# Kernel optimization log

Measured on AMD Instinct MI355X. Metric: run time of the kernel, lower is better.

## Reference

```python
import jax, jax.numpy as jnp
import numpy as np

B, S, D = 4, 2048, 1024
H = 16
HS = D // H  # 64


def setup_inputs() -> dict:
    key = jax.random.key(0)
    ks = jax.random.split(key, 6)
    scale = 1.0 / np.sqrt(D)
    x = jax.random.normal(ks[0], (B, S, D), dtype=jnp.float32)
    # per-head projection weights, stacked: [H, D, HS]
    Wq = jax.random.normal(ks[1], (H, D, HS), dtype=jnp.float32) * scale
    Wk = jax.random.normal(ks[2], (H, D, HS), dtype=jnp.float32) * scale
    Wv = jax.random.normal(ks[3], (H, D, HS), dtype=jnp.float32) * scale
    Wo = jax.random.normal(ks[4], (D, D), dtype=jnp.float32) * scale
    bo = jax.random.normal(ks[5], (D,), dtype=jnp.float32) * 0.01
    return {"x": x, "Wq": Wq, "Wk": Wk, "Wv": Wv, "Wo": Wo, "bo": bo}


def reference(x, Wq, Wk, Wv, Wo, bo):
    # Per-head dense projections (no bias): [B,S,D] x [H,D,HS] -> [B,H,S,HS]
    q = jnp.einsum('bsd,hde->bhse', x, Wq)
    k = jnp.einsum('bsd,hde->bhse', x, Wk)
    v = jnp.einsum('bsd,hde->bhse', x, Wv)
    # scaled dot-product scores: [B,H,S,S]
    scores = jnp.einsum('bhse,bhte->bhst', q, k) / jnp.sqrt(jnp.asarray(HS, dtype=x.dtype))
    # causal mask (lower triangular kept)
    causal = jnp.tril(jnp.ones((S, S), dtype=bool))
    scores = jnp.where(causal, scores, -jnp.inf)
    attn = jax.nn.softmax(scores, axis=-1)
    # dropout is identity at inference (rate handled as 0)
    out = jnp.einsum('bhst,bhte->bhse', attn, v)  # [B,H,S,HS]
    # concat heads: [B,S,H*HS] = [B,S,D]
    out = jnp.transpose(out, (0, 2, 1, 3)).reshape(B, S, D)
    return out @ Wo + bo
```

## Files before the change

kernel.cpp:

```cpp
#include <hip/hip_runtime.h>
#include <hip/hip_bf16.h>
#include <stdint.h>

#define NB 4
#define NS 2048
#define ND 1024
#define NH 16
#define NHS 64
#define NEG_BIG (-1e30f)
#define Q_SCALE 0.18033688011112042f

typedef __bf16 bf16x8 __attribute__((ext_vector_type(8)));
typedef float floatx4 __attribute__((ext_vector_type(4)));
typedef short s16x4 __attribute__((ext_vector_type(4)));

#if defined(__has_builtin)
#if __has_builtin(__builtin_amdgcn_mfma_f32_16x16x16bf16_1k)
#define HAVE_MFMA1K 1
#endif
#endif
#ifndef HAVE_MFMA1K
#define HAVE_MFMA1K 0
#endif

static constexpr size_t WSLAB = (size_t)NH * ND * NHS;
static constexpr size_t QSLAB = (size_t)NB * NH * NS * NHS;
static constexpr size_t XSLAB = (size_t)NB * NS * ND;

__device__ __forceinline__ uint16_t f2b(float f) {
    union { __hip_bfloat16 h; uint16_t u; } cv;
    cv.h = __float2bfloat16(f);
    return cv.u;
}

__device__ __forceinline__ void gll16(const void* g, void* l) {
  __builtin_amdgcn_global_load_lds(
      (__attribute__((address_space(1))) void*)(uintptr_t)g,
      (__attribute__((address_space(3))) void*)(uintptr_t)l,
      16, 0, 0);
}

__global__ __launch_bounds__(256) void k_prep(
    const float* __restrict__ x, const float* __restrict__ Wq,
    const float* __restrict__ Wk, const float* __restrict__ Wv,
    const float* __restrict__ Wo, uint16_t* __restrict__ xb,
    uint16_t* __restrict__ wt) {
  __shared__ __align__(16) uint16_t T[64][72];
  int bid = blockIdx.x;
  int tid = threadIdx.x;
  if (bid < 4096) {
    size_t i0 = ((size_t)bid * 256 + tid) * 8;
    float4 f0 = *(const float4*)&x[i0];
    float4 f1 = *(const float4*)&x[i0 + 4];
    __align__(16) uint16_t tmp[8];
    tmp[0] = f2b(f0.x); tmp[1] = f2b(f0.y); tmp[2] = f2b(f0.z); tmp[3] = f2b(f0.w);
    tmp[4] = f2b(f1.x); tmp[5] = f2b(f1.y); tmp[6] = f2b(f1.z); tmp[7] = f2b(f1.w);
    *(uint4*)&xb[i0] = *(uint4*)tmp;
    return;
  }
  bid -= 4096;
  const float* src; uint16_t* dst;
  int srcStride, dstStride, r0, c0;
  if (bid < 768) {
    int mat = bid >> 8;
    int rem = bid & 255;
    int h = rem >> 4, dt = rem & 15;
    const float* W = (mat == 0) ? Wq : (mat == 1) ? Wk : Wv;
    src = W + (size_t)h * (ND * NHS);
    dst = wt + (size_t)mat * WSLAB + (size_t)h * (NHS * ND);
    srcStride = NHS; dstStride = ND;
    r0 = dt * 64; c0 = 0;
  } else {
    int rem = bid - 768;
    int dt = rem >> 4, et = rem & 15;
    src = Wo; dst = wt + 3 * WSLAB;
    srcStride = ND; dstStride = ND;
    r0 = dt * 64; c0 = et * 64;
  }
  for (int u = tid; u < 1024; u += 256) {
    int row = u >> 4, cq = u & 15;
    float4 f = *(const float4*)&src[(size_t)(r0 + row) * srcStride + c0 + cq * 4];
    uint16_t* p = &T[row][cq * 4];
    p[0] = f2b(f.x); p[1] = f2b(f.y); p[2] = f2b(f.z); p[3] = f2b(f.w);
  }
  __syncthreads();
  for (int u = tid; u < 512; u += 256) {
    int c = u >> 3, cg = u & 7;
    __align__(16) uint16_t tmp[8];
    for (int j = 0; j < 8; j++) tmp[j] = T[cg * 8 + j][c];
    *(uint4*)&dst[(size_t)(c0 + c) * dstStride + r0 + cg * 8] = *(uint4*)tmp;
  }
}

__global__ __launch_bounds__(512, 2) void k_qkv(
    const uint16_t* __restrict__ xb, const uint16_t* __restrict__ wt,
    uint16_t* __restrict__ qk, uint16_t* __restrict__ vt) {
  __shared__ __align__(16) uint16_t L[8 * 8704];

  int bid = blockIdx.x;
  int xcd = bid & 7, idx = bid >> 3;
  int mt = xcd * 4 + (idx & 3);
  int ntile = idx >> 2;
  int m0 = mt * 256;
  int n0 = ntile * 256;

  int tid = threadIdx.x;
  int wave = tid >> 6, lane = tid & 63, quad = lane >> 4, l16 = lane & 15;
  int wr = wave >> 2, wc = wave & 3;

  const uint16_t* pA = xb + (size_t)(m0 + (tid >> 2)) * ND + (tid & 3) * 8;
  const uint16_t* pB = wt + (size_t)(n0 + (tid >> 2)) * ND + (tid & 3) * 8;
  const int ldsStageOff = wave * 512;

  const int offA = (wr * 128 + l16) * 32 + quad * 8;
  const int offB = (wc * 64 + l16) * 32 + quad * 8;

  floatx4 acc[8][4];
  #pragma unroll
  for (int i = 0; i < 8; i++)
    #pragma unroll
    for (int j = 0; j < 4; j++) acc[i][j] = (floatx4){0.f, 0.f, 0.f, 0.f};

#define STAGE(H)                                                                \
  do {                                                                          \
    int h_ = (H);                                                               \
    if (h_ < 64) {                                                              \
      const uint16_t* g_ = ((h_ & 1) ? pB : pA) + (h_ >> 2) * 64 + ((h_ >> 1) & 1) * 32; \
      uint16_t* l_ = &L[(h_ & 7) * 8704 + ldsStageOff];                         \
      gll16(g_, l_);                                                            \
      gll16(g_ + 128 * ND, l_ + 4096);                                          \
    }                                                                           \
  } while (0)

#define PH_BAR()                         \
  do {                                   \
    asm volatile("" ::: "memory");       \
    __builtin_amdgcn_s_barrier();        \
    asm volatile("" ::: "memory");       \
  } while (0)

  STAGE(0); STAGE(1); STAGE(2); STAGE(3); STAGE(4); STAGE(5);
  asm volatile("s_waitcnt vmcnt(4)" ::: "memory");
  PH_BAR();

  bf16x8 bfr[4];

#define MFMA16(QM)                                                                                   \
  acc[(QM)*4+0][0] = __builtin_amdgcn_mfma_f32_16x16x32_bf16(af0_, bfr[0], acc[(QM)*4+0][0],0,0,0);  \
  acc[(QM)*4+0][1] = __builtin_amdgcn_mfma_f32_16x16x32_bf16(af0_, bfr[1], acc[(QM)*4+0][1],0,0,0);  \
  acc[(QM)*4+0][2] = __builtin_amdgcn_mfma_f32_16x16x32_bf16(af0_, bfr[2], acc[(QM)*4+0][2],0,0,0);  \
  acc[(QM)*4+0][3] = __builtin_amdgcn_mfma_f32_16x16x32_bf16(af0_, bfr[3], acc[(QM)*4+0][3],0,0,0);  \
  acc[(QM)*4+1][0] = __builtin_amdgcn_mfma_f32_16x16x32_bf16(af1_, bfr[0], acc[(QM)*4+1][0],0,0,0);  \
  acc[(QM)*4+1][1] = __builtin_amdgcn_mfma_f32_16x16x32_bf16(af1_, bfr[1], acc[(QM)*4+1][1],0,0,0);  \
  acc[(QM)*4+1][2] = __builtin_amdgcn_mfma_f32_16x16x32_bf16(af1_, bfr[2], acc[(QM)*4+1][2],0,0,0);  \
  acc[(QM)*4+1][3] = __builtin_amdgcn_mfma_f32_16x16x32_bf16(af1_, bfr[3], acc[(QM)*4+1][3],0,0,0);  \
  acc[(QM)*4+2][0] = __builtin_amdgcn_mfma_f32_16x16x32_bf16(af2_, bfr[0], acc[(QM)*4+2][0],0,0,0);  \
  acc[(QM)*4+2][1] = __builtin_amdgcn_mfma_f32_16x16x32_bf16(af2_, bfr[1], acc[(QM)*4+2][1],0,0,0);  \
  acc[(QM)*4+2][2] = __builtin_amdgcn_mfma_f32_16x16x32_bf16(af2_, bfr[2], acc[(QM)*4+2][2],0,0,0);  \
  acc[(QM)*4+2][3] = __builtin_amdgcn_mfma_f32_16x16x32_bf16(af2_, bfr[3], acc[(QM)*4+2][3],0,0,0);  \
  acc[(QM)*4+3][0] = __builtin_amdgcn_mfma_f32_16x16x32_bf16(af3_, bfr[0], acc[(QM)*4+3][0],0,0,0);  \
  acc[(QM)*4+3][1] = __builtin_amdgcn_mfma_f32_16x16x32_bf16(af3_, bfr[1], acc[(QM)*4+3][1],0,0,0);  \
  acc[(QM)*4+3][2] = __builtin_amdgcn_mfma_f32_16x16x32_bf16(af3_, bfr[2], acc[(QM)*4+3][2],0,0,0);  \
  acc[(QM)*4+3][3] = __builtin_amdgcn_mfma_f32_16x16x32_bf16(af3_, bfr[3], acc[(QM)*4+3][3],0,0,0)

#define PHASE(T4, KK, QM, HSTAGE, LOADB)                                        \
  {                                                                             \
    const int slA_ = (((T4) + 2 * (KK)) & 7) * 8704;                            \
    bf16x8 af0_ = *(const bf16x8*)&L[slA_ + offA + (QM) * 2048 + 0 * 512];      \
    bf16x8 af1_ = *(const bf16x8*)&L[slA_ + offA + (QM) * 2048 + 1 * 512];      \
    bf16x8 af2_ = *(const bf16x8*)&L[slA_ + offA + (QM) * 2048 + 2 * 512];      \
    bf16x8 af3_ = *(const bf16x8*)&L[slA_ + offA + (QM) * 2048 + 3 * 512];      \
    if (LOADB) {                                                                \
      const int slB_ = (((T4) + 2 * (KK) + 1) & 7) * 8704;                      \
      bfr[0] = *(const bf16x8*)&L[slB_ + offB + 0 * 512];                       \
      bfr[1] = *(const bf16x8*)&L[slB_ + offB + 1 * 512];                       \
      bfr[2] = *(const bf16x8*)&L[slB_ + offB + 2 * 512];                       \
      bfr[3] = *(const bf16x8*)&L[slB_ + offB + 3 * 512];                       \
    }                                                                           \
    STAGE(HSTAGE);                                                              \
    PH_BAR();                                                                   \
    __builtin_amdgcn_s_setprio(1);                                              \
    MFMA16(QM);                                                                 \
    __builtin_amdgcn_s_setprio(0);                                              \
  }

  for (int t = 0; t < 16; ++t) {
    int t4 = t * 4;
    PHASE(t4, 0, 0, t4 + 6, 1);
    PH_BAR();
    PHASE(t4, 0, 1, t4 + 7, 0);
    PH_BAR();
    PHASE(t4, 1, 0, t4 + 8, 1);
    PH_BAR();
    PHASE(t4, 1, 1, t4 + 9, 0);
    if (t < 14)       { asm volatile("s_waitcnt vmcnt(4)" ::: "memory"); }
    else if (t == 14) { asm volatile("s_waitcnt vmcnt(0)" ::: "memory"); }
    PH_BAR();
  }
#undef PHASE
#undef MFMA16
#undef STAGE
#undef PH_BAR

  int matid = n0 >> 10;
  if (matid == 2) {
    uint16_t* wbuf = &L[wave * 8704];
    #pragma unroll
    for (int mq = 0; mq < 8; mq++)
      #pragma unroll
      for (int nt = 0; nt < 4; nt++) {
        __align__(8) uint16_t t4v[4];
        #pragma unroll
        for (int r = 0; r < 4; r++) t4v[r] = f2b(acc[mq][nt][r]);
        int e = nt * 16 + l16;
        *(uint2*)&wbuf[e * 136 + mq * 16 + quad * 4] = *(uint2*)t4v;
      }
    __syncthreads();
    int hb = (n0 - 2048) >> 6;
    int b = m0 >> 11, s0m = m0 & 2047;
    #pragma unroll
    for (int i = 0; i < 16; i++) {
      int c = i * 512 + tid;
      int row = c >> 5, sb = c & 31;
      int hl = row >> 6, e = row & 63;
      int wsrc = (sb >> 4) * 4 + hl;
      uint4 d = *(const uint4*)&L[wsrc * 8704 + e * 136 + (sb & 15) * 8];
      *(uint4*)&vt[((size_t)(b * 16 + hb + hl) * 64 + e) * 2048 + s0m + sb * 8] = d;
    }
  } else {
    float scale = (matid == 0) ? Q_SCALE : 1.0f;
    uint16_t* base = qk + (size_t)matid * QSLAB;
    int hh = ((n0 & 1023) >> 6) + wc;
    #pragma unroll
    for (int mq = 0; mq < 8; mq++) {
      int m = m0 + wr * 128 + mq * 16 + quad * 4;
      int b = m >> 11, s = m & 2047;
      size_t rbase = ((size_t)(b * 16 + hh) * NS + s) * NHS;
      #pragma unroll
      for (int nt = 0; nt < 4; nt++)
        #pragma unroll
        for (int r = 0; r < 4; r++)
          base[rbase + (size_t)r * NHS + nt * 16 + l16] = f2b(acc[mq][nt][r] * scale);
    }
  }
}

#if HAVE_MFMA1K
__global__ __launch_bounds__(256, 4) void k_attn(
    const uint16_t* __restrict__ Q, const uint16_t* __restrict__ K,
    const uint16_t* __restrict__ VT, uint16_t* __restrict__ Y) {
  __shared__ __align__(16) uint16_t Ks[64][72];
  __shared__ __align__(16) uint16_t Vs[64][72];
  int bh = blockIdx.y;
  int b = bh >> 4, h = bh & 15;
  int ta = blockIdx.x;
  int tb = 31 - ta;
  const uint16_t* Qp = Q + (size_t)bh * (NS * NHS);
  const uint16_t* Kp = K + (size_t)bh * (NS * NHS);
  const uint16_t* Vp = VT + (size_t)bh * (NS * NHS);
  int tid = threadIdx.x;
  int wv = tid >> 6, lane = tid & 63, quad = lane >> 4, l16 = lane & 15;

  int row0 = tid >> 3, cg0 = tid & 7;
  int row1 = (tid + 256) >> 3, cg1 = tid & 7;

  int rA = ta * 64 + wv * 16 + l16;
  int rB = tb * 64 + wv * 16 + l16;
  bf16x8 aqA0 = *(const bf16x8*)&Qp[(size_t)rA * NHS + quad * 8];
  bf16x8 aqA1 = *(const bf16x8*)&Qp[(size_t)rA * NHS + 32 + quad * 8];
  bf16x8 aqB0 = *(const bf16x8*)&Qp[(size_t)rB * NHS + quad * 8];
  bf16x8 aqB1 = *(const bf16x8*)&Qp[(size_t)rB * NHS + 32 + quad * 8];

  float lAs = 0.f, lBs = 0.f;
  floatx4 oA[4], oB[4];
  for (int et = 0; et < 4; et++) {
    oA[et] = (floatx4){0.f, 0.f, 0.f, 0.f};
    oB[et] = (floatx4){0.f, 0.f, 0.f, 0.f};
  }

  uint4 rk0, rk1, rv0, rv1;
  rk0 = *(const uint4*)&Kp[(size_t)(0 * 64 + row0) * NHS + cg0 * 8];
  rk1 = *(const uint4*)&Kp[(size_t)(0 * 64 + row1) * NHS + cg1 * 8];
  rv0 = *(const uint4*)&Vp[(size_t)row0 * NS + 0 * 64 + cg0 * 8];
  rv1 = *(const uint4*)&Vp[(size_t)row1 * NS + 0 * 64 + cg1 * 8];

  for (int kt = 0; kt <= tb; kt++) {
    bool doA = (kt <= ta);
    __syncthreads();
    *(uint4*)&Ks[row0][cg0 * 8] = rk0;
    *(uint4*)&Ks[row1][cg1 * 8] = rk1;
    *(uint4*)&Vs[row0][cg0 * 8] = rv0;
    *(uint4*)&Vs[row1][cg1 * 8] = rv1;
    __syncthreads();
    if (kt < tb) {
      rk0 = *(const uint4*)&Kp[(size_t)((kt + 1) * 64 + row0) * NHS + cg0 * 8];
      rk1 = *(const uint4*)&Kp[(size_t)((kt + 1) * 64 + row1) * NHS + cg1 * 8];
      rv0 = *(const uint4*)&Vp[(size_t)row0 * NS + (kt + 1) * 64 + cg0 * 8];
      rv1 = *(const uint4*)&Vp[(size_t)row1 * NS + (kt + 1) * 64 + cg1 * 8];
    }

    s16x4 pbA[4], pbB[4];
    for (int ct = 0; ct < 4; ct++) {
      bf16x8 kb0 = *(const bf16x8*)&Ks[ct * 16 + l16][quad * 8];
      bf16x8 kb1 = *(const bf16x8*)&Ks[ct * 16 + l16][32 + quad * 8];
      int key = kt * 64 + ct * 16 + quad * 4;
      floatx4 c = (floatx4){0.f, 0.f, 0.f, 0.f};
      c = __builtin_amdgcn_mfma_f32_16x16x32_bf16(kb0, aqB0, c, 0, 0, 0);
      c = __builtin_amdgcn_mfma_f32_16x16x32_bf16(kb1, aqB1, c, 0, 0, 0);
      for (int r = 0; r < 4; r++) {
        float s = (kt == tb && key + r > rB) ? NEG_BIG : c[r];
        float p = __builtin_amdgcn_exp2f(s);
        lBs += p;
        pbB[ct][r] = (short)f2b(p);
      }
      if (doA) {
        floatx4 d = (floatx4){0.f, 0.f, 0.f, 0.f};
        d = __builtin_amdgcn_mfma_f32_16x16x32_bf16(kb0, aqA0, d, 0, 0, 0);
        d = __builtin_amdgcn_mfma_f32_16x16x32_bf16(kb1, aqA1, d, 0, 0, 0);
        for (int r = 0; r < 4; r++) {
          float s = (kt == ta && key + r > rA) ? NEG_BIG : d[r];
          float p = __builtin_amdgcn_exp2f(s);
          lAs += p;
          pbA[ct][r] = (short)f2b(p);
        }
      }
    }
    for (int et = 0; et < 4; et++)
      for (int ct = 0; ct < 4; ct++) {
        s16x4 va = *(const s16x4*)&Vs[et * 16 + l16][ct * 16 + quad * 4];
        oB[et] = __builtin_amdgcn_mfma_f32_16x16x16bf16_1k(va, pbB[ct], oB[et], 0, 0, 0);
        if (doA)
          oA[et] = __builtin_amdgcn_mfma_f32_16x16x16bf16_1k(va, pbA[ct], oA[et], 0, 0, 0);
      }
  }
  lAs += __shfl_xor(lAs, 16, 64); lAs += __shfl_xor(lAs, 32, 64);
  lBs += __shfl_xor(lBs, 16, 64); lBs += __shfl_xor(lBs, 32, 64);
  float invA = 1.f / lAs, invB = 1.f / lBs;
  uint16_t* yb = Y + (size_t)b * NS * ND + (size_t)h * NHS;
  for (int et = 0; et < 4; et++) {
    __align__(8) uint16_t tA[4], tB[4];
    for (int r = 0; r < 4; r++) {
      tA[r] = f2b(oA[et][r] * invA);
      tB[r] = f2b(oB[et][r] * invB);
    }
    *(uint2*)&yb[(size_t)rA * ND + et * 16 + quad * 4] = *(uint2*)tA;
    *(uint2*)&yb[(size_t)rB * ND + et * 16 + quad * 4] = *(uint2*)tB;
  }
}
#else
__global__ __launch_bounds__(256) void k_attn(
    const uint16_t* __restrict__ Q, const uint16_t* __restrict__ K,
    const uint16_t* __restrict__ VT, uint16_t* __restrict__ Y) {
  __shared__ __align__(16) uint16_t Ks[64][72];
  __shared__ __align__(16) uint16_t Vs[64][72];
  __shared__ __align__(16) uint16_t Ps[4][2][16][72];
  int bh = blockIdx.y;
  int b = bh >> 4, h = bh & 15;
  int ta = blockIdx.x;
  int tb = 31 - ta;
  const uint16_t* Qp = Q + (size_t)bh * (NS * NHS);
  const uint16_t* Kp = K + (size_t)bh * (NS * NHS);
  const uint16_t* Vp = VT + (size_t)bh * (NS * NHS);
  int tid = threadIdx.x;
  int wv = tid >> 6, lane = tid & 63, quad = lane >> 4, l16 = lane & 15;

  int rA = ta * 64 + wv * 16 + l16;
  int rB = tb * 64 + wv * 16 + l16;
  bf16x8 aqA0 = *(const bf16x8*)&Qp[(size_t)rA * NHS + quad * 8];
  bf16x8 aqA1 = *(const bf16x8*)&Qp[(size_t)rA * NHS + 32 + quad * 8];
  bf16x8 aqB0 = *(const bf16x8*)&Qp[(size_t)rB * NHS + quad * 8];
  bf16x8 aqB1 = *(const bf16x8*)&Qp[(size_t)rB * NHS + 32 + quad * 8];

  float lA[4] = {0.f, 0.f, 0.f, 0.f}, lB[4] = {0.f, 0.f, 0.f, 0.f};
  floatx4 oA[4], oB[4];
  for (int ct = 0; ct < 4; ct++) {
    oA[ct] = (floatx4){0.f, 0.f, 0.f, 0.f};
    oB[ct] = (floatx4){0.f, 0.f, 0.f, 0.f};
  }
  for (int kt = 0; kt <= tb; kt++) {
    bool doA = (kt <= ta);
    __syncthreads();
    for (int u = tid; u < 512; u += 256) {
      int row = u >> 3, cg = u & 7;
      *(uint4*)&Ks[row][cg * 8] =
          *(const uint4*)&Kp[(size_t)(kt * 64 + row) * NHS + cg * 8];
    }
    for (int u = tid; u < 512; u += 256) {
      int row = u >> 3, cg = u & 7;
      *(uint4*)&Vs[row][cg * 8] =
          *(const uint4*)&Vp[(size_t)row * NS + kt * 64 + cg * 8];
    }
    __syncthreads();
    floatx4 sA[4], sB[4];
    for (int ct = 0; ct < 4; ct++) {
      bf16x8 kb0 = *(const bf16x8*)&Ks[ct * 16 + l16][quad * 8];
      bf16x8 kb1 = *(const bf16x8*)&Ks[ct * 16 + l16][32 + quad * 8];
      floatx4 c = (floatx4){0.f, 0.f, 0.f, 0.f};
      c = __builtin_amdgcn_mfma_f32_16x16x32_bf16(aqB0, kb0, c, 0, 0, 0);
      c = __builtin_amdgcn_mfma_f32_16x16x32_bf16(aqB1, kb1, c, 0, 0, 0);
      sB[ct] = c;
      if (doA) {
        floatx4 d = (floatx4){0.f, 0.f, 0.f, 0.f};
        d = __builtin_amdgcn_mfma_f32_16x16x32_bf16(aqA0, kb0, d, 0, 0, 0);
        d = __builtin_amdgcn_mfma_f32_16x16x32_bf16(aqA1, kb1, d, 0, 0, 0);
        sA[ct] = d;
      }
    }
    if (kt == tb) {
      int qrb = tb * 64 + wv * 16 + quad * 4;
      for (int ct = 0; ct < 4; ct++) {
        int kg = kt * 64 + ct * 16 + l16;
        for (int r = 0; r < 4; r++)
          sB[ct][r] = (kg <= qrb + r) ? sB[ct][r] : NEG_BIG;
      }
    }
    if (doA && kt == ta) {
      int qrb = ta * 64 + wv * 16 + quad * 4;
      for (int ct = 0; ct < 4; ct++) {
        int kg = kt * 64 + ct * 16 + l16;
        for (int r = 0; r < 4; r++)
          sA[ct][r] = (kg <= qrb + r) ? sA[ct][r] : NEG_BIG;
      }
    }
    for (int ct = 0; ct < 4; ct++)
      for (int r = 0; r < 4; r++) {
        float p = __builtin_amdgcn_exp2f(sB[ct][r]);
        lB[r] += p;
        Ps[wv][1][quad * 4 + r][ct * 16 + l16] = f2b(p);
      }
    if (doA)
      for (int ct = 0; ct < 4; ct++)
        for (int r = 0; r < 4; r++) {
          float p = __builtin_amdgcn_exp2f(sA[ct][r]);
          lA[r] += p;
          Ps[wv][0][quad * 4 + r][ct * 16 + l16] = f2b(p);
        }
    bf16x8 apB0 = *(const bf16x8*)&Ps[wv][1][l16][quad * 8];
    bf16x8 apB1 = *(const bf16x8*)&Ps[wv][1][l16][32 + quad * 8];
    bf16x8 apA0, apA1;
    if (doA) {
      apA0 = *(const bf16x8*)&Ps[wv][0][l16][quad * 8];
      apA1 = *(const bf16x8*)&Ps[wv][0][l16][32 + quad * 8];
    }
    for (int ct = 0; ct < 4; ct++) {
      bf16x8 vb0 = *(const bf16x8*)&Vs[ct * 16 + l16][quad * 8];
      bf16x8 vb1 = *(const bf16x8*)&Vs[ct * 16 + l16][32 + quad * 8];
      oB[ct] = __builtin_amdgcn_mfma_f32_16x16x32_bf16(apB0, vb0, oB[ct], 0, 0, 0);
      oB[ct] = __builtin_amdgcn_mfma_f32_16x16x32_bf16(apB1, vb1, oB[ct], 0, 0, 0);
      if (doA) {
        oA[ct] = __builtin_amdgcn_mfma_f32_16x16x32_bf16(apA0, vb0, oA[ct], 0, 0, 0);
        oA[ct] = __builtin_amdgcn_mfma_f32_16x16x32_bf16(apA1, vb1, oA[ct], 0, 0, 0);
      }
    }
  }
  for (int off = 1; off < 16; off <<= 1)
    for (int r = 0; r < 4; r++) {
      lA[r] += __shfl_xor(lA[r], off, 64);
      lB[r] += __shfl_xor(lB[r], off, 64);
    }
  uint16_t* yb = Y + (size_t)b * NS * ND + (size_t)h * NHS;
  for (int ct = 0; ct < 4; ct++)
    for (int r = 0; r < 4; r++) {
      int sA_ = ta * 64 + wv * 16 + quad * 4 + r;
      int sB_ = tb * 64 + wv * 16 + quad * 4 + r;
      yb[(size_t)sA_ * ND + ct * 16 + l16] = f2b(oA[ct][r] / lA[r]);
      yb[(size_t)sB_ * ND + ct * 16 + l16] = f2b(oB[ct][r] / lB[r]);
    }
}
#endif

__global__ __launch_bounds__(256) void k_proj(
    const uint16_t* __restrict__ y, const uint16_t* __restrict__ wot,
    const float* __restrict__ bo, float* __restrict__ out) {
  __shared__ __align__(16) uint16_t As[128 * 64];
  __shared__ __align__(16) uint16_t Bs[128 * 64];
  int m0 = blockIdx.x * 128;
  int n0 = blockIdx.y * 128;
  int tid = threadIdx.x;
  int wv = tid >> 6, lane = tid & 63, quad = lane >> 4, l16 = lane & 15;
  int wr = wv >> 1, wc = wv & 1;
  int srow = lane >> 3, scol = lane & 7;

  floatx4 acc[4][4];
  for (int i = 0; i < 4; i++)
    for (int j = 0; j < 4; j++) acc[i][j] = (floatx4){0.f, 0.f, 0.f, 0.f};

  for (int k0 = 0; k0 < ND; k0 += 64) {
    __syncthreads();
    for (int j = 0; j < 4; j++) {
      int rg = wv * 4 + j;
      int r = rg * 8 + srow;
      gll16(&y[(size_t)(m0 + r) * ND + k0 + scol * 8], &As[rg * 512]);
      gll16(&wot[(size_t)(n0 + r) * ND + k0 + scol * 8], &Bs[rg * 512]);
    }
    __syncthreads();
    for (int kk = 0; kk < 2; kk++) {
      bf16x8 af[4], bfr[4];
      for (int t = 0; t < 4; t++) {
        af[t]  = *(const bf16x8*)&As[(wr * 64 + t * 16 + l16) * 64 + kk * 32 + quad * 8];
        bfr[t] = *(const bf16x8*)&Bs[(wc * 64 + t * 16 + l16) * 64 + kk * 32 + quad * 8];
      }
      for (int mt = 0; mt < 4; mt++)
        for (int nt = 0; nt < 4; nt++)
          acc[mt][nt] = __builtin_amdgcn_mfma_f32_16x16x32_bf16(af[mt], bfr[nt], acc[mt][nt], 0, 0, 0);
    }
  }
  for (int mt = 0; mt < 4; mt++)
    for (int nt = 0; nt < 4; nt++)
      for (int r = 0; r < 4; r++) {
        int s = m0 + wr * 64 + mt * 16 + quad * 4 + r;
        int n = n0 + wc * 64 + nt * 16 + l16;
        out[(size_t)s * ND + n] = acc[mt][nt][r] + bo[n];
      }
}

extern "C" void kernel_launch(void* const* d_in, const int* in_sizes, int n_in,
                              void* d_out, int out_size, void* d_ws, size_t ws_size,
                              hipStream_t stream) {
  const float* x  = (const float*)d_in[0];
  const float* Wq = (const float*)d_in[1];
  const float* Wk = (const float*)d_in[2];
  const float* Wv = (const float*)d_in[3];
  const float* Wo = (const float*)d_in[4];
  const float* bo = (const float*)d_in[5];
  uint16_t* ws = (uint16_t*)d_ws;

  uint16_t* wt = ws;
  uint16_t* xb = ws + 4 * WSLAB;
  uint16_t* q  = xb + XSLAB;
  uint16_t* k  = q + QSLAB;
  uint16_t* vt = k + QSLAB;
  uint16_t* y  = vt + QSLAB;

  k_prep<<<dim3(5120), dim3(256), 0, stream>>>(x, Wq, Wk, Wv, Wo, xb, wt);
  k_qkv<<<dim3(384), dim3(512), 0, stream>>>(xb, wt, q, vt);
  k_attn<<<dim3(16, NB * NH), dim3(256), 0, stream>>>(q, k, vt, y);
  k_proj<<<dim3(64, 8), dim3(256), 0, stream>>>(y, wt + 3 * WSLAB, bo, (float*)d_out);
}
```

Before: 263.5 us.

## Shrink QKV GEMM LDS ring to four stages and store V transpose directly

Cuts the k_qkv shared-memory staging ring from 8 padded slots to 4 unpadded slots and rewrites the prefetch schedule and waitcnt points to match, so the pipeline is shallower. It also raises the launch-bounds occupancy hint from 2 to 4 blocks per CU, and the V output now goes straight from registers to global memory as 8-byte stores instead of being transposed through LDS. The aim is higher occupancy and a cheaper V epilogue. The risks are less latency hiding from the shallower prefetch, LDS bank conflicts now that the padding is gone, and uncoalesced 8-byte V stores.

```diff
diff --git a/kernel.cpp b/kernel.cpp
--- a/kernel.cpp
+++ b/kernel.cpp
@@ -92,10 +92,10 @@
   }
 }
 
-__global__ __launch_bounds__(512, 2) void k_qkv(
+__global__ __launch_bounds__(512, 4) void k_qkv(
     const uint16_t* __restrict__ xb, const uint16_t* __restrict__ wt,
     uint16_t* __restrict__ qk, uint16_t* __restrict__ vt) {
-  __shared__ __align__(16) uint16_t L[8 * 8704];
+  __shared__ __align__(16) uint16_t L[4 * 8192];
 
   int bid = blockIdx.x;
   int xcd = bid & 7, idx = bid >> 3;
@@ -126,7 +126,7 @@
     int h_ = (H);                                                               \
     if (h_ < 64) {                                                              \
       const uint16_t* g_ = ((h_ & 1) ? pB : pA) + (h_ >> 2) * 64 + ((h_ >> 1) & 1) * 32; \
-      uint16_t* l_ = &L[(h_ & 7) * 8704 + ldsStageOff];                         \
+      uint16_t* l_ = &L[(h_ & 3) * 8192 + ldsStageOff];                         \
       gll16(g_, l_);                                                            \
       gll16(g_ + 128 * ND, l_ + 4096);                                          \
     }                                                                           \
@@ -139,7 +139,7 @@
     asm volatile("" ::: "memory");       \
   } while (0)
 
-  STAGE(0); STAGE(1); STAGE(2); STAGE(3); STAGE(4); STAGE(5);
+  STAGE(0); STAGE(1); STAGE(2); STAGE(3);
   asm volatile("s_waitcnt vmcnt(4)" ::: "memory");
   PH_BAR();
 
@@ -163,21 +163,19 @@
   acc[(QM)*4+3][2] = __builtin_amdgcn_mfma_f32_16x16x32_bf16(af3_, bfr[2], acc[(QM)*4+3][2],0,0,0);  \
   acc[(QM)*4+3][3] = __builtin_amdgcn_mfma_f32_16x16x32_bf16(af3_, bfr[3], acc[(QM)*4+3][3],0,0,0)
 
-#define PHASE(T4, KK, QM, HSTAGE, LOADB)                                        \
+#define PHASE(SLOTA, SLOTB, QM, HSTAGE, LOADB, DOSTAGE)                         \
   {                                                                             \
-    const int slA_ = (((T4) + 2 * (KK)) & 7) * 8704;                            \
-    bf16x8 af0_ = *(const bf16x8*)&L[slA_ + offA + (QM) * 2048 + 0 * 512];      \
-    bf16x8 af1_ = *(const bf16x8*)&L[slA_ + offA + (QM) * 2048 + 1 * 512];      \
-    bf16x8 af2_ = *(const bf16x8*)&L[slA_ + offA + (QM) * 2048 + 2 * 512];      \
-    bf16x8 af3_ = *(const bf16x8*)&L[slA_ + offA + (QM) * 2048 + 3 * 512];      \
+    bf16x8 af0_ = *(const bf16x8*)&L[(SLOTA) + offA + (QM) * 2048 + 0 * 512];   \
+    bf16x8 af1_ = *(const bf16x8*)&L[(SLOTA) + offA + (QM) * 2048 + 1 * 512];   \
+    bf16x8 af2_ = *(const bf16x8*)&L[(SLOTA) + offA + (QM) * 2048 + 2 * 512];   \
+    bf16x8 af3_ = *(const bf16x8*)&L[(SLOTA) + offA + (QM) * 2048 + 3 * 512];   \
     if (LOADB) {                                                                \
-      const int slB_ = (((T4) + 2 * (KK) + 1) & 7) * 8704;                      \
-      bfr[0] = *(const bf16x8*)&L[slB_ + offB + 0 * 512];                       \
-      bfr[1] = *(const bf16x8*)&L[slB_ + offB + 1 * 512];                       \
-      bfr[2] = *(const bf16x8*)&L[slB_ + offB + 2 * 512];                       \
-      bfr[3] = *(const bf16x8*)&L[slB_ + offB + 3 * 512];                       \
+      bfr[0] = *(const bf16x8*)&L[(SLOTB) + offB + 0 * 512];                    \
+      bfr[1] = *(const bf16x8*)&L[(SLOTB) + offB + 1 * 512];                    \
+      bfr[2] = *(const bf16x8*)&L[(SLOTB) + offB + 2 * 512];                    \
+      bfr[3] = *(const bf16x8*)&L[(SLOTB) + offB + 3 * 512];                    \
     }                                                                           \
-    STAGE(HSTAGE);                                                              \
+    if (DOSTAGE) STAGE(HSTAGE);                                                 \
     PH_BAR();                                                                   \
     __builtin_amdgcn_s_setprio(1);                                              \
     MFMA16(QM);                                                                 \
@@ -186,15 +184,16 @@
 
   for (int t = 0; t < 16; ++t) {
     int t4 = t * 4;
-    PHASE(t4, 0, 0, t4 + 6, 1);
+    PHASE(0, 8192, 0, t4 + 2, 1, (t > 0));
     PH_BAR();
-    PHASE(t4, 0, 1, t4 + 7, 0);
+    PHASE(0, 8192, 1, t4 + 5, 0, 1);
+    if (t < 15) { asm volatile("s_waitcnt vmcnt(2)" ::: "memory"); }
+    else        { asm volatile("s_waitcnt vmcnt(0)" ::: "memory"); }
     PH_BAR();
-    PHASE(t4, 1, 0, t4 + 8, 1);
+    PHASE(16384, 24576, 0, t4 + 4, 1, 1);
     PH_BAR();
-    PHASE(t4, 1, 1, t4 + 9, 0);
-    if (t < 14)       { asm volatile("s_waitcnt vmcnt(4)" ::: "memory"); }
-    else if (t == 14) { asm volatile("s_waitcnt vmcnt(0)" ::: "memory"); }
+    PHASE(16384, 24576, 1, t4 + 7, 0, 1);
+    if (t < 15) { asm volatile("s_waitcnt vmcnt(2)" ::: "memory"); }
     PH_BAR();
   }
 #undef PHASE
@@ -204,28 +203,20 @@
 
   int matid = n0 >> 10;
   if (matid == 2) {
-    uint16_t* wbuf = &L[wave * 8704];
+    int hh = ((n0 - 2048) >> 6) + wc;
+    int b = m0 >> 11;
+    int sbase = (m0 & 2047) + wr * 128;
     #pragma unroll
-    for (int mq = 0; mq < 8; mq++)
+    for (int nt = 0; nt < 4; nt++) {
+      int e = nt * 16 + l16;
+      uint16_t* vrow = vt + ((size_t)(b * 16 + hh) * 64 + e) * NS;
       #pragma unroll
-      for (int nt = 0; nt < 4; nt++) {
+      for (int mq = 0; mq < 8; mq++) {
         __align__(8) uint16_t t4v[4];
         #pragma unroll
         for (int r = 0; r < 4; r++) t4v[r] = f2b(acc[mq][nt][r]);
-        int e = nt * 16 + l16;
-        *(uint2*)&wbuf[e * 136 + mq * 16 + quad * 4] = *(uint2*)t4v;
-      }
-    __syncthreads();
-    int hb = (n0 - 2048) >> 6;
-    int b = m0 >> 11, s0m = m0 & 2047;
-    #pragma unroll
-    for (int i = 0; i < 16; i++) {
-      int c = i * 512 + tid;
-      int row = c >> 5, sb = c & 31;
-      int hl = row >> 6, e = row & 63;
-      int wsrc = (sb >> 4) * 4 + hl;
-      uint4 d = *(const uint4*)&L[wsrc * 8704 + e * 136 + (sb & 15) * 8];
-      *(uint4*)&vt[((size_t)(b * 16 + hb + hl) * 64 + e) * 2048 + s0m + sb * 8] = d;
+        *(uint2*)&vrow[sbase + mq * 16 + quad * 4] = *(uint2*)t4v;
+      }
     }
   } else {
     float scale = (matid == 0) ? Q_SCALE : 1.0f;
```

Result: slower. 730.3 us (+177.1%).
